# Kernel tuning notes

Measured on AMD Instinct MI355X. Metric: run time of the kernel, lower is better.

The kernel has to match this reference:

```python
import jax, jax.numpy as jnp
import numpy as np

N, H, W = 8, 512, 512
C = 16
TEX = 1024
LEVELS = 4
SH_START = 3


def setup_inputs() -> dict:
    key = jax.random.key(0)
    ks = jax.random.split(key, 2 + LEVELS)
    d = {
        "uv_map": jax.random.uniform(ks[0], (N, H, W, 2), dtype=jnp.float32),
        "sh_basis_map": jax.random.normal(ks[1], (N, H, W, 9), dtype=jnp.float32),
    }
    for i in range(LEVELS):
        s = int(round(TEX / 2.0 ** i))
        d[f"tex{i}"] = jax.random.normal(ks[2 + i], (s, s, C), dtype=jnp.float32) * 0.05
    return d


def _grid_sample_bilinear(tex, uv):
    """torch.grid_sample(mode=bilinear, padding=zeros, align_corners=False),
    grid built as (2u-1, -(2v-1)). tex: [Ht,Wt,C]; uv: [N,H,W,2] in [0,1].
    Returns [N,H,W,C]."""
    Ht, Wt, _ = tex.shape
    gx = uv[..., 0] * 2.0 - 1.0
    gy = -(uv[..., 1] * 2.0 - 1.0)  # y flip from original code
    ix = ((gx + 1.0) * Wt - 1.0) * 0.5  # unnormalize, align_corners=False
    iy = ((gy + 1.0) * Ht - 1.0) * 0.5
    ix0 = jnp.floor(ix); iy0 = jnp.floor(iy)
    ix1 = ix0 + 1.0;     iy1 = iy0 + 1.0
    wx1 = ix - ix0; wx0 = 1.0 - wx1
    wy1 = iy - iy0; wy0 = 1.0 - wy1

    def gather(iyf, ixf):
        iyi = iyf.astype(jnp.int32)
        ixi = ixf.astype(jnp.int32)
        valid = ((iyi >= 0) & (iyi < Ht) & (ixi >= 0) & (ixi < Wt))
        v = tex[jnp.clip(iyi, 0, Ht - 1), jnp.clip(ixi, 0, Wt - 1)]  # [N,H,W,C]
        return v * valid[..., None].astype(tex.dtype)  # zeros padding

    out = (gather(iy0, ix0) * (wy0 * wx0)[..., None]
           + gather(iy0, ix1) * (wy0 * wx1)[..., None]
           + gather(iy1, ix0) * (wy1 * wx0)[..., None]
           + gather(iy1, ix1) * (wy1 * wx1)[..., None])
    return out


def reference(uv_map, sh_basis_map, tex0, tex1, tex2, tex3):
    # accumulate all mipmap levels sampled at the same uv grid
    out = _grid_sample_bilinear(tex0, uv_map)
    for tex in (tex1, tex2, tex3):
        out = out + _grid_sample_bilinear(tex, uv_map)
    # mask pixels where u == 0
    mask = (uv_map[..., 0] == 0.0)[..., None]
    out = jnp.where(mask, 0.0, out)
    # SH multiply on channels [SH_START : SH_START+9]
    out = jnp.concatenate(
        [out[..., :SH_START],
         out[..., SH_START:SH_START + 9] * sh_basis_map,
         out[..., SH_START + 9:]], axis=-1)
    return out.transpose(0, 3, 1, 2)  # [N, C, H, W]
```

## Files before the change

kernel.cpp:

```cpp
#include <hip/hip_runtime.h>

#define NB 8
#define H 512
#define W 512
#define HW (H * W)
#define C 16
#define NPIX (NB * HW)
#define SH_START 3

#define G 32
#define NBINS (G * G)
#define CAP 4096
#define DUMPSLOT (NBINS * CAP)

#define BS_BLOCKS 256
#define BS_THREADS 1024
#define PXB (NPIX / BS_BLOCKS)
#define KPT (PXB / BS_THREADS)

#define OFF_RECS   ((size_t)0)
#define OFF_INTER  ((size_t)67112960)
#define OFF_CUR    ((size_t)134221824)
#define WS_NEED    ((size_t)134225920)

#define TSTR 20
#define LDS0 0
#define LDS1 (1156 * TSTR)
#define LDS2 ((1156 + 324) * TSTR)
#define LDS3 ((1156 + 324 + 100) * TSTR)
#define LDS_FLOATS ((1156 + 324 + 100 + 36) * TSTR)

typedef float f32x4 __attribute__((ext_vector_type(4)));
typedef unsigned int u32x2 __attribute__((ext_vector_type(2)));

__device__ __forceinline__ int bin_of(float u, float v) {
    int bx = (int)(u * (float)G);
    int by = (int)(v * (float)G);
    bx = bx < 0 ? 0 : (bx > G - 1 ? G - 1 : bx);
    by = by < 0 ? 0 : (by > G - 1 ? G - 1 : by);
    return by * G + bx;
}

__device__ __forceinline__ unsigned int f2bf(float f) {
    unsigned int u = __float_as_uint(f);
    unsigned int r = (u + 0x7FFFu + ((u >> 16) & 1u)) >> 16;
    return r & 0xFFFFu;
}

__global__ __launch_bounds__(BS_THREADS) void binsort_kernel(const float* __restrict__ uv,
                                                             int* __restrict__ cur,
                                                             float4* __restrict__ recs) {
    __shared__ f32x4 stage[PXB];
    __shared__ int h[NBINS];
    __shared__ int lstart[NBINS];
    __shared__ int gbase[NBINS];
    int tid = threadIdx.x;
    int pbase = blockIdx.x * PXB;
    const float2* uv2 = reinterpret_cast<const float2*>(uv);

    float2 p[KPT];
    int bn[KPT];
    h[tid] = 0;
    __syncthreads();
#pragma unroll
    for (int k = 0; k < KPT; ++k) {
        p[k] = uv2[pbase + tid + k * BS_THREADS];
        bn[k] = bin_of(p[k].x, p[k].y);
        atomicAdd(&h[bn[k]], 1);
    }
    __syncthreads();
    int cnt = h[tid];
    gbase[tid] = atomicAdd(&cur[tid], cnt);
    lstart[tid] = cnt;
    __syncthreads();
    for (int off = 1; off < NBINS; off <<= 1) {
        int v = (tid >= off) ? lstart[tid - off] : 0;
        __syncthreads();
        lstart[tid] += v;
        __syncthreads();
    }
    int excl = lstart[tid] - cnt;
    __syncthreads();
    lstart[tid] = excl;
    h[tid] = 0;
    __syncthreads();
#pragma unroll
    for (int k = 0; k < KPT; ++k) {
        int b = bn[k];
        int r = atomicAdd(&h[b], 1);
        int ls = lstart[b] + r;
        int within = gbase[b] + r;
        int gs = (within < CAP) ? (b * CAP + within) : DUMPSLOT;
        f32x4 rec;
        rec.x = p[k].x;
        rec.y = p[k].y;
        rec.z = __int_as_float(pbase + tid + k * BS_THREADS);
        rec.w = __int_as_float(gs);
        stage[ls] = rec;
    }
    __syncthreads();
#pragma unroll
    for (int k = 0; k < KPT; ++k) {
        f32x4 rec = stage[tid + k * BS_THREADS];
        int gs = __float_as_int(rec.w);
        __builtin_nontemporal_store(rec, reinterpret_cast<f32x4*>(recs) + gs);
    }
}

template<int S, int N>
__device__ __forceinline__ void stage_mip(const float* __restrict__ t,
                                          float* __restrict__ lbase,
                                          int x0, int y0, int tid) {
    for (int i = tid; i < N * N * 4; i += 1024) {
        int tx = i >> 2, ch = i & 3;
        int ly = tx / N, lx = tx - ly * N;
        int gy = y0 + ly, gx = x0 + lx;
        f32x4 val = {0.0f, 0.0f, 0.0f, 0.0f};
        if (gy >= 0 && gy < S && gx >= 0 && gx < S)
            val = *reinterpret_cast<const f32x4*>(t + ((size_t)(gy * S + gx)) * C + ch * 4);
        *reinterpret_cast<f32x4*>(lbase + (ly * N + lx) * TSTR + ch * 4) = val;
    }
}

template<int S, int N>
__device__ __forceinline__ void sample_mip_lds(const float* __restrict__ lbase,
                                               int x0, int y0,
                                               float u, float v, int ch4, f32x4& acc) {
    float Sf = (float)S;
    float gx = u * 2.0f - 1.0f;
    float gy = -(v * 2.0f - 1.0f);
    float ix = ((gx + 1.0f) * Sf - 1.0f) * 0.5f;
    float iy = ((gy + 1.0f) * Sf - 1.0f) * 0.5f;
    float ix0f = floorf(ix);
    float iy0f = floorf(iy);
    float wx1 = ix - ix0f;
    float wy1 = iy - iy0f;
    float wx0 = 1.0f - wx1;
    float wy0 = 1.0f - wy1;
    int lx = (int)ix0f - x0;
    int ly = (int)iy0f - y0;
    const float* p = lbase + (ly * N + lx) * TSTR + ch4;
    f32x4 t00 = *reinterpret_cast<const f32x4*>(p);
    f32x4 t01 = *reinterpret_cast<const f32x4*>(p + TSTR);
    f32x4 t10 = *reinterpret_cast<const f32x4*>(p + TSTR * N);
    f32x4 t11 = *reinterpret_cast<const f32x4*>(p + TSTR * N + TSTR);
    float w00 = wy0 * wx0, w01 = wy0 * wx1, w10 = wy1 * wx0, w11 = wy1 * wx1;
    acc.x = fmaf(t00.x, w00, acc.x);
    acc.y = fmaf(t00.y, w00, acc.y);
    acc.z = fmaf(t00.z, w00, acc.z);
    acc.w = fmaf(t00.w, w00, acc.w);
    acc.x = fmaf(t01.x, w01, acc.x);
    acc.y = fmaf(t01.y, w01, acc.y);
    acc.z = fmaf(t01.z, w01, acc.z);
    acc.w = fmaf(t01.w, w01, acc.w);
    acc.x = fmaf(t10.x, w10, acc.x);
    acc.y = fmaf(t10.y, w10, acc.y);
    acc.z = fmaf(t10.z, w10, acc.z);
    acc.w = fmaf(t10.w, w10, acc.w);
    acc.x = fmaf(t11.x, w11, acc.x);
    acc.y = fmaf(t11.y, w11, acc.y);
    acc.z = fmaf(t11.z, w11, acc.z);
    acc.w = fmaf(t11.w, w11, acc.w);
}

__global__ __launch_bounds__(1024) void phaseA_kernel(
    const float4* __restrict__ recs, const int* __restrict__ cur,
    const float* __restrict__ t0, const float* __restrict__ t1,
    const float* __restrict__ t2, const float* __restrict__ t3,
    unsigned int* __restrict__ inter) {
    __shared__ float lds[LDS_FLOATS];
    int blk = blockIdx.x;
    int bin = (blk & 7) * (NBINS / 8) + (blk >> 3);
    int bx = bin & (G - 1), by = bin >> 5;
    int tid = threadIdx.x;

    const int x0_0 = bx * 32 - 1, y0_0 = 1024 - (by + 1) * 32 - 1;
    const int x0_1 = bx * 16 - 1, y0_1 = 512  - (by + 1) * 16 - 1;
    const int x0_2 = bx * 8  - 1, y0_2 = 256  - (by + 1) * 8  - 1;
    const int x0_3 = bx * 4  - 1, y0_3 = 128  - (by + 1) * 4  - 1;

    stage_mip<1024, 34>(t0, lds + LDS0, x0_0, y0_0, tid);
    stage_mip<512,  18>(t1, lds + LDS1, x0_1, y0_1, tid);
    stage_mip<256,  10>(t2, lds + LDS2, x0_2, y0_2, tid);
    stage_mip<128,   6>(t3, lds + LDS3, x0_3, y0_3, tid);
    __syncthreads();

    int start = bin * CAP;
    int cnt = cur[bin];
    if (cnt > CAP) cnt = CAP;

    int wave = tid >> 6;
    int lane = tid & 63;
    int q    = lane >> 2;
    int chq  = lane & 3;
    int ch4  = chq * 4;

    for (int i0 = wave * 16; i0 < cnt; i0 += 16 * 16) {
        int i = i0 + q;
        if (i < cnt) {
            float4 r = recs[start + i];
            float u = r.x, v = r.y;
            int pix = __float_as_int(r.z);

            f32x4 acc = {0.0f, 0.0f, 0.0f, 0.0f};
            sample_mip_lds<1024, 34>(lds + LDS0, x0_0, y0_0, u, v, ch4, acc);
            sample_mip_lds<512,  18>(lds + LDS1, x0_1, y0_1, u, v, ch4, acc);
            sample_mip_lds<256,  10>(lds + LDS2, x0_2, y0_2, u, v, ch4, acc);
            sample_mip_lds<128,   6>(lds + LDS3, x0_3, y0_3, u, v, ch4, acc);

            if (u == 0.0f) acc = (f32x4){0.0f, 0.0f, 0.0f, 0.0f};

            u32x2 pk;
            pk.x = f2bf(acc.x) | (f2bf(acc.y) << 16);
            pk.y = f2bf(acc.z) | (f2bf(acc.w) << 16);
            u32x2* op = reinterpret_cast<u32x2*>(inter) + (size_t)pix * 4 + chq;
            __builtin_nontemporal_store(pk, op);
        }
    }
}

__global__ __launch_bounds__(256) void phaseB_kernel(const unsigned int* __restrict__ inter,
                                                     const float* __restrict__ sh,
                                                     float* __restrict__ out) {
    __shared__ float shs[256 * 9];
    int base = blockIdx.x * 256;
    const float* shp = sh + (size_t)base * 9;
    for (int i = threadIdx.x; i < 256 * 9; i += 256) shs[i] = shp[i];
    __syncthreads();

    int pix = base + threadIdx.x;
    const uint4* ip = reinterpret_cast<const uint4*>(inter) + (size_t)pix * 2;
    uint4 a = ip[0];
    uint4 b = ip[1];
#define BLO(x) __uint_as_float((x) << 16)
#define BHI(x) __uint_as_float((x) & 0xFFFF0000u)
    float c0  = BLO(a.x), c1  = BHI(a.x), c2  = BLO(a.y), c3  = BHI(a.y);
    float c4  = BLO(a.z), c5  = BHI(a.z), c6  = BLO(a.w), c7  = BHI(a.w);
    float c8  = BLO(b.x), c9  = BHI(b.x), c10 = BLO(b.y), c11 = BHI(b.y);
    float c12 = BLO(b.z), c13 = BHI(b.z), c14 = BLO(b.w), c15 = BHI(b.w);
#undef BLO
#undef BHI
    const float* s = &shs[threadIdx.x * 9];
    c3  *= s[0];
    c4  *= s[1]; c5  *= s[2]; c6  *= s[3]; c7  *= s[4];
    c8  *= s[5]; c9  *= s[6]; c10 *= s[7]; c11 *= s[8];

    int n  = pix >> 18;
    int hw = pix & (HW - 1);
    float* op = out + (size_t)n * C * HW + hw;
    __builtin_nontemporal_store(c0,  op + 0 * HW);
    __builtin_nontemporal_store(c1,  op + 1 * HW);
    __builtin_nontemporal_store(c2,  op + 2 * HW);
    __builtin_nontemporal_store(c3,  op + 3 * HW);
    __builtin_nontemporal_store(c4,  op + 4 * HW);
    __builtin_nontemporal_store(c5,  op + 5 * HW);
    __builtin_nontemporal_store(c6,  op + 6 * HW);
    __builtin_nontemporal_store(c7,  op + 7 * HW);
    __builtin_nontemporal_store(c8,  op + (size_t)8 * HW);
    __builtin_nontemporal_store(c9,  op + (size_t)9 * HW);
    __builtin_nontemporal_store(c10, op + (size_t)10 * HW);
    __builtin_nontemporal_store(c11, op + (size_t)11 * HW);
    __builtin_nontemporal_store(c12, op + (size_t)12 * HW);
    __builtin_nontemporal_store(c13, op + (size_t)13 * HW);
    __builtin_nontemporal_store(c14, op + (size_t)14 * HW);
    __builtin_nontemporal_store(c15, op + (size_t)15 * HW);
}

__device__ __forceinline__ void tap(const float* __restrict__ t, int S, int iy, int ix,
                                    float w, float acc[C]) {
    if (iy >= 0 && iy < S && ix >= 0 && ix < S) {
        const float4* p = reinterpret_cast<const float4*>(t + ((size_t)iy * S + ix) * C);
        float4 q0 = p[0];
        float4 q1 = p[1];
        float4 q2 = p[2];
        float4 q3 = p[3];
        acc[0]  = fmaf(q0.x, w, acc[0]);
        acc[1]  = fmaf(q0.y, w, acc[1]);
        acc[2]  = fmaf(q0.z, w, acc[2]);
        acc[3]  = fmaf(q0.w, w, acc[3]);
        acc[4]  = fmaf(q1.x, w, acc[4]);
        acc[5]  = fmaf(q1.y, w, acc[5]);
        acc[6]  = fmaf(q1.z, w, acc[6]);
        acc[7]  = fmaf(q1.w, w, acc[7]);
        acc[8]  = fmaf(q2.x, w, acc[8]);
        acc[9]  = fmaf(q2.y, w, acc[9]);
        acc[10] = fmaf(q2.z, w, acc[10]);
        acc[11] = fmaf(q2.w, w, acc[11]);
        acc[12] = fmaf(q3.x, w, acc[12]);
        acc[13] = fmaf(q3.y, w, acc[13]);
        acc[14] = fmaf(q3.z, w, acc[14]);
        acc[15] = fmaf(q3.w, w, acc[15]);
    }
}

__device__ __forceinline__ void sample_level(const float* __restrict__ t, int S,
                                             float u, float v, float acc[C]) {
    float Sf = (float)S;
    float gx = u * 2.0f - 1.0f;
    float gy = -(v * 2.0f - 1.0f);
    float ix = ((gx + 1.0f) * Sf - 1.0f) * 0.5f;
    float iy = ((gy + 1.0f) * Sf - 1.0f) * 0.5f;
    float ix0f = floorf(ix);
    float iy0f = floorf(iy);
    float wx1 = ix - ix0f;
    float wy1 = iy - iy0f;
    float wx0 = 1.0f - wx1;
    float wy0 = 1.0f - wy1;
    int ix0 = (int)ix0f;
    int iy0 = (int)iy0f;
    tap(t, S, iy0,     ix0,     wy0 * wx0, acc);
    tap(t, S, iy0,     ix0 + 1, wy0 * wx1, acc);
    tap(t, S, iy0 + 1, ix0,     wy1 * wx0, acc);
    tap(t, S, iy0 + 1, ix0 + 1, wy1 * wx1, acc);
}

__global__ __launch_bounds__(256) void texmap_kernel(
    const float* __restrict__ uv, const float* __restrict__ sh,
    const float* __restrict__ t0, const float* __restrict__ t1,
    const float* __restrict__ t2, const float* __restrict__ t3,
    float* __restrict__ out) {
    int idx = blockIdx.x * 256 + threadIdx.x;
    if (idx >= NPIX) return;

    float2 uvv = *reinterpret_cast<const float2*>(uv + (size_t)idx * 2);
    float u = uvv.x;
    float v = uvv.y;

    float acc[C];
#pragma unroll
    for (int c = 0; c < C; ++c) acc[c] = 0.0f;

    sample_level(t0, 1024, u, v, acc);
    sample_level(t1, 512,  u, v, acc);
    sample_level(t2, 256,  u, v, acc);
    sample_level(t3, 128,  u, v, acc);

    if (u == 0.0f) {
#pragma unroll
        for (int c = 0; c < C; ++c) acc[c] = 0.0f;
    }

    const float* shp = sh + (size_t)idx * 9;
#pragma unroll
    for (int j = 0; j < 9; ++j) acc[SH_START + j] *= shp[j];

    int n  = idx >> 18;
    int hw = idx & (HW - 1);
    float* op = out + (size_t)n * C * HW + hw;
#pragma unroll
    for (int c = 0; c < C; ++c) {
        __builtin_nontemporal_store(acc[c], op + (size_t)c * HW);
    }
}

extern "C" void kernel_launch(void* const* d_in, const int* in_sizes, int n_in,
                              void* d_out, int out_size, void* d_ws, size_t ws_size,
                              hipStream_t stream) {
    const float* uv = (const float*)d_in[0];
    const float* sh = (const float*)d_in[1];
    const float* t0 = (const float*)d_in[2];
    const float* t1 = (const float*)d_in[3];
    const float* t2 = (const float*)d_in[4];
    const float* t3 = (const float*)d_in[5];
    float* out = (float*)d_out;

    if (ws_size < WS_NEED) {
        texmap_kernel<<<dim3((NPIX + 255) / 256), dim3(256), 0, stream>>>(
            uv, sh, t0, t1, t2, t3, out);
        return;
    }

    char* ws = (char*)d_ws;
    float4*       recs  = (float4*)(ws + OFF_RECS);
    unsigned int* inter = (unsigned int*)(ws + OFF_INTER);
    int*          cur   = (int*)(ws + OFF_CUR);

    (void)hipMemsetAsync(cur, 0, NBINS * sizeof(int), stream);
    binsort_kernel<<<dim3(BS_BLOCKS), dim3(BS_THREADS), 0, stream>>>(uv, cur, recs);
    phaseA_kernel<<<dim3(NBINS), dim3(1024), 0, stream>>>(
        recs, cur, t0, t1, t2, t3, inter);
    phaseB_kernel<<<dim3(NPIX / 256), dim3(256), 0, stream>>>(inter, sh, out);
}
```

Before: 177.6 us.

## Use finer 64x64 UV bins with smaller LDS tiles and 512-thread sampling blocks

Doubles the bin grid resolution to 64x64. Each sampling block now stages a much smaller texture footprint per mip level into shared memory, and uses 512 threads instead of 1024 so more blocks can be resident per CU. The binsort kernel is generalized so each thread handles several bins in the histogram and scan, and it launches twice as many blocks. The trade-off is 4x more bins, more scan work and atomics in binsort, and a lower per-bin capacity of 1024 that risks overflow into the dump slot if bins are uneven.

```diff
diff --git a/kernel.cpp b/kernel.cpp
--- a/kernel.cpp
+++ b/kernel.cpp
@@ -8,12 +8,12 @@
 #define NPIX (NB * HW)
 #define SH_START 3
 
-#define G 32
+#define G 64
 #define NBINS (G * G)
-#define CAP 4096
+#define CAP 1024
 #define DUMPSLOT (NBINS * CAP)
 
-#define BS_BLOCKS 256
+#define BS_BLOCKS 512
 #define BS_THREADS 1024
 #define PXB (NPIX / BS_BLOCKS)
 #define KPT (PXB / BS_THREADS)
@@ -21,14 +21,18 @@
 #define OFF_RECS   ((size_t)0)
 #define OFF_INTER  ((size_t)67112960)
 #define OFF_CUR    ((size_t)134221824)
-#define WS_NEED    ((size_t)134225920)
-
-#define TSTR 20
+#define WS_NEED    ((size_t)134238208)
+
+#define TSTR 16
+#define NT0 18
+#define NT1 10
+#define NT2 6
+#define NT3 4
 #define LDS0 0
-#define LDS1 (1156 * TSTR)
-#define LDS2 ((1156 + 324) * TSTR)
-#define LDS3 ((1156 + 324 + 100) * TSTR)
-#define LDS_FLOATS ((1156 + 324 + 100 + 36) * TSTR)
+#define LDS1 (324 * TSTR)
+#define LDS2 ((324 + 100) * TSTR)
+#define LDS3 ((324 + 100 + 36) * TSTR)
+#define LDS_FLOATS ((324 + 100 + 36 + 16) * TSTR)
 
 typedef float f32x4 __attribute__((ext_vector_type(4)));
 typedef unsigned int u32x2 __attribute__((ext_vector_type(2)));
@@ -60,7 +64,8 @@
 
     float2 p[KPT];
     int bn[KPT];
-    h[tid] = 0;
+#pragma unroll
+    for (int j = 0; j < NBINS / BS_THREADS; ++j) h[tid + j * BS_THREADS] = 0;
     __syncthreads();
 #pragma unroll
     for (int k = 0; k < KPT; ++k) {
@@ -69,20 +74,34 @@
         atomicAdd(&h[bn[k]], 1);
     }
     __syncthreads();
-    int cnt = h[tid];
-    gbase[tid] = atomicAdd(&cur[tid], cnt);
-    lstart[tid] = cnt;
+    int cnt_[NBINS / BS_THREADS];
+#pragma unroll
+    for (int j = 0; j < NBINS / BS_THREADS; ++j) {
+        int b = tid + j * BS_THREADS;
+        cnt_[j] = h[b];
+        gbase[b] = atomicAdd(&cur[b], cnt_[j]);
+        lstart[b] = cnt_[j];
+    }
     __syncthreads();
     for (int off = 1; off < NBINS; off <<= 1) {
-        int v = (tid >= off) ? lstart[tid - off] : 0;
+        int tmp[NBINS / BS_THREADS];
+#pragma unroll
+        for (int j = 0; j < NBINS / BS_THREADS; ++j) {
+            int b = tid + j * BS_THREADS;
+            tmp[j] = (b >= off) ? lstart[b - off] : 0;
+        }
         __syncthreads();
-        lstart[tid] += v;
+#pragma unroll
+        for (int j = 0; j < NBINS / BS_THREADS; ++j)
+            lstart[tid + j * BS_THREADS] += tmp[j];
         __syncthreads();
     }
-    int excl = lstart[tid] - cnt;
-    __syncthreads();
-    lstart[tid] = excl;
-    h[tid] = 0;
+#pragma unroll
+    for (int j = 0; j < NBINS / BS_THREADS; ++j) {
+        int b = tid + j * BS_THREADS;
+        lstart[b] -= cnt_[j];
+        h[b] = 0;
+    }
     __syncthreads();
 #pragma unroll
     for (int k = 0; k < KPT; ++k) {
@@ -111,7 +130,7 @@
 __device__ __forceinline__ void stage_mip(const float* __restrict__ t,
                                           float* __restrict__ lbase,
                                           int x0, int y0, int tid) {
-    for (int i = tid; i < N * N * 4; i += 1024) {
+    for (int i = tid; i < N * N * 4; i += 512) {
         int tx = i >> 2, ch = i & 3;
         int ly = tx / N, lx = tx - ly * N;
         int gy = y0 + ly, gx = x0 + lx;
@@ -163,7 +182,7 @@
     acc.w = fmaf(t11.w, w11, acc.w);
 }
 
-__global__ __launch_bounds__(1024) void phaseA_kernel(
+__global__ __launch_bounds__(512, 8) void phaseA_kernel(
     const float4* __restrict__ recs, const int* __restrict__ cur,
     const float* __restrict__ t0, const float* __restrict__ t1,
     const float* __restrict__ t2, const float* __restrict__ t3,
@@ -171,18 +190,18 @@
     __shared__ float lds[LDS_FLOATS];
     int blk = blockIdx.x;
     int bin = (blk & 7) * (NBINS / 8) + (blk >> 3);
-    int bx = bin & (G - 1), by = bin >> 5;
+    int bx = bin & (G - 1), by = bin >> 6;
     int tid = threadIdx.x;
 
-    const int x0_0 = bx * 32 - 1, y0_0 = 1024 - (by + 1) * 32 - 1;
-    const int x0_1 = bx * 16 - 1, y0_1 = 512  - (by + 1) * 16 - 1;
-    const int x0_2 = bx * 8  - 1, y0_2 = 256  - (by + 1) * 8  - 1;
-    const int x0_3 = bx * 4  - 1, y0_3 = 128  - (by + 1) * 4  - 1;
-
-    stage_mip<1024, 34>(t0, lds + LDS0, x0_0, y0_0, tid);
-    stage_mip<512,  18>(t1, lds + LDS1, x0_1, y0_1, tid);
-    stage_mip<256,  10>(t2, lds + LDS2, x0_2, y0_2, tid);
-    stage_mip<128,   6>(t3, lds + LDS3, x0_3, y0_3, tid);
+    const int x0_0 = bx * 16 - 1, y0_0 = 1024 - (by + 1) * 16 - 1;
+    const int x0_1 = bx * 8  - 1, y0_1 = 512  - (by + 1) * 8  - 1;
+    const int x0_2 = bx * 4  - 1, y0_2 = 256  - (by + 1) * 4  - 1;
+    const int x0_3 = bx * 2  - 1, y0_3 = 128  - (by + 1) * 2  - 1;
+
+    stage_mip<1024, NT0>(t0, lds + LDS0, x0_0, y0_0, tid);
+    stage_mip<512,  NT1>(t1, lds + LDS1, x0_1, y0_1, tid);
+    stage_mip<256,  NT2>(t2, lds + LDS2, x0_2, y0_2, tid);
+    stage_mip<128,  NT3>(t3, lds + LDS3, x0_3, y0_3, tid);
     __syncthreads();
 
     int start = bin * CAP;
@@ -195,7 +214,7 @@
     int chq  = lane & 3;
     int ch4  = chq * 4;
 
-    for (int i0 = wave * 16; i0 < cnt; i0 += 16 * 16) {
+    for (int i0 = wave * 16; i0 < cnt; i0 += 8 * 16) {
         int i = i0 + q;
         if (i < cnt) {
             float4 r = recs[start + i];
@@ -203,10 +222,10 @@
             int pix = __float_as_int(r.z);
 
             f32x4 acc = {0.0f, 0.0f, 0.0f, 0.0f};
-            sample_mip_lds<1024, 34>(lds + LDS0, x0_0, y0_0, u, v, ch4, acc);
-            sample_mip_lds<512,  18>(lds + LDS1, x0_1, y0_1, u, v, ch4, acc);
-            sample_mip_lds<256,  10>(lds + LDS2, x0_2, y0_2, u, v, ch4, acc);
-            sample_mip_lds<128,   6>(lds + LDS3, x0_3, y0_3, u, v, ch4, acc);
+            sample_mip_lds<1024, NT0>(lds + LDS0, x0_0, y0_0, u, v, ch4, acc);
+            sample_mip_lds<512,  NT1>(lds + LDS1, x0_1, y0_1, u, v, ch4, acc);
+            sample_mip_lds<256,  NT2>(lds + LDS2, x0_2, y0_2, u, v, ch4, acc);
+            sample_mip_lds<128,  NT3>(lds + LDS3, x0_3, y0_3, u, v, ch4, acc);
 
             if (u == 0.0f) acc = (f32x4){0.0f, 0.0f, 0.0f, 0.0f};
 
@@ -377,7 +396,7 @@
 
     (void)hipMemsetAsync(cur, 0, NBINS * sizeof(int), stream);
     binsort_kernel<<<dim3(BS_BLOCKS), dim3(BS_THREADS), 0, stream>>>(uv, cur, recs);
-    phaseA_kernel<<<dim3(NBINS), dim3(1024), 0, stream>>>(
+    phaseA_kernel<<<dim3(NBINS), dim3(512), 0, stream>>>(
         recs, cur, t0, t1, t2, t3, inter);
     phaseB_kernel<<<dim3(NPIX / 256), dim3(256), 0, stream>>>(inter, sh, out);
 }
```

Result: slower. 215.4 us (+21.3%).

## Stage mip tiles in LDS as bf16, halve phaseA block size, prefetch records

Applied to the files above, without the earlier changes.

Texture tiles staged into LDS are converted to packed bf16 with an 8-dword texel stride, which halves LDS footprint and read bandwidth. PhaseA blocks drop from 1024 to 512 threads, so more blocks can be resident per CU. The sampling loop is software-pipelined so the next record is loaded while the current one is sampled, and the bin count is read before staging. Quantising the texels to bf16 before interpolation adds precision error on top of the existing bf16 intermediate.

```diff
diff --git a/kernel.cpp b/kernel.cpp
--- a/kernel.cpp
+++ b/kernel.cpp
@@ -23,12 +23,11 @@
 #define OFF_CUR    ((size_t)134221824)
 #define WS_NEED    ((size_t)134225920)
 
-#define TSTR 20
-#define LDS0 0
-#define LDS1 (1156 * TSTR)
-#define LDS2 ((1156 + 324) * TSTR)
-#define LDS3 ((1156 + 324 + 100) * TSTR)
-#define LDS_FLOATS ((1156 + 324 + 100 + 36) * TSTR)
+#define D0 0
+#define D1 (1156 * 8)
+#define D2 ((1156 + 324) * 8)
+#define D3 ((1156 + 324 + 100) * 8)
+#define LDS_DWORDS ((1156 + 324 + 100 + 36) * 8)
 
 typedef float f32x4 __attribute__((ext_vector_type(4)));
 typedef unsigned int u32x2 __attribute__((ext_vector_type(2)));
@@ -108,24 +107,30 @@
 }
 
 template<int S, int N>
-__device__ __forceinline__ void stage_mip(const float* __restrict__ t,
-                                          float* __restrict__ lbase,
-                                          int x0, int y0, int tid) {
-    for (int i = tid; i < N * N * 4; i += 1024) {
+__device__ __forceinline__ void stage_mip_bf16(const float* __restrict__ t,
+                                               unsigned int* __restrict__ lbase,
+                                               int x0, int y0, int tid) {
+    for (int i = tid; i < N * N * 4; i += 512) {
         int tx = i >> 2, ch = i & 3;
         int ly = tx / N, lx = tx - ly * N;
         int gy = y0 + ly, gx = x0 + lx;
-        f32x4 val = {0.0f, 0.0f, 0.0f, 0.0f};
-        if (gy >= 0 && gy < S && gx >= 0 && gx < S)
-            val = *reinterpret_cast<const f32x4*>(t + ((size_t)(gy * S + gx)) * C + ch * 4);
-        *reinterpret_cast<f32x4*>(lbase + (ly * N + lx) * TSTR + ch * 4) = val;
-    }
-}
+        u32x2 d = {0u, 0u};
+        if (gy >= 0 && gy < S && gx >= 0 && gx < S) {
+            f32x4 val = *reinterpret_cast<const f32x4*>(t + ((size_t)(gy * S + gx)) * C + ch * 4);
+            d.x = f2bf(val.x) | (f2bf(val.y) << 16);
+            d.y = f2bf(val.z) | (f2bf(val.w) << 16);
+        }
+        *reinterpret_cast<u32x2*>(lbase + (ly * N + lx) * 8 + ch * 2) = d;
+    }
+}
+
+#define BFL(x) __uint_as_float((x) << 16)
+#define BFH(x) __uint_as_float((x) & 0xFFFF0000u)
 
 template<int S, int N>
-__device__ __forceinline__ void sample_mip_lds(const float* __restrict__ lbase,
-                                               int x0, int y0,
-                                               float u, float v, int ch4, f32x4& acc) {
+__device__ __forceinline__ void sample_mip_bf16(const unsigned int* __restrict__ lbase,
+                                                int x0, int y0,
+                                                float u, float v, int ch2, f32x4& acc) {
     float Sf = (float)S;
     float gx = u * 2.0f - 1.0f;
     float gy = -(v * 2.0f - 1.0f);
@@ -139,83 +144,95 @@
     float wy0 = 1.0f - wy1;
     int lx = (int)ix0f - x0;
     int ly = (int)iy0f - y0;
-    const float* p = lbase + (ly * N + lx) * TSTR + ch4;
-    f32x4 t00 = *reinterpret_cast<const f32x4*>(p);
-    f32x4 t01 = *reinterpret_cast<const f32x4*>(p + TSTR);
-    f32x4 t10 = *reinterpret_cast<const f32x4*>(p + TSTR * N);
-    f32x4 t11 = *reinterpret_cast<const f32x4*>(p + TSTR * N + TSTR);
+    const unsigned int* p = lbase + (ly * N + lx) * 8 + ch2;
+    u32x2 d00 = *reinterpret_cast<const u32x2*>(p);
+    u32x2 d01 = *reinterpret_cast<const u32x2*>(p + 8);
+    u32x2 d10 = *reinterpret_cast<const u32x2*>(p + 8 * N);
+    u32x2 d11 = *reinterpret_cast<const u32x2*>(p + 8 * N + 8);
     float w00 = wy0 * wx0, w01 = wy0 * wx1, w10 = wy1 * wx0, w11 = wy1 * wx1;
-    acc.x = fmaf(t00.x, w00, acc.x);
-    acc.y = fmaf(t00.y, w00, acc.y);
-    acc.z = fmaf(t00.z, w00, acc.z);
-    acc.w = fmaf(t00.w, w00, acc.w);
-    acc.x = fmaf(t01.x, w01, acc.x);
-    acc.y = fmaf(t01.y, w01, acc.y);
-    acc.z = fmaf(t01.z, w01, acc.z);
-    acc.w = fmaf(t01.w, w01, acc.w);
-    acc.x = fmaf(t10.x, w10, acc.x);
-    acc.y = fmaf(t10.y, w10, acc.y);
-    acc.z = fmaf(t10.z, w10, acc.z);
-    acc.w = fmaf(t10.w, w10, acc.w);
-    acc.x = fmaf(t11.x, w11, acc.x);
-    acc.y = fmaf(t11.y, w11, acc.y);
-    acc.z = fmaf(t11.z, w11, acc.z);
-    acc.w = fmaf(t11.w, w11, acc.w);
-}
-
-__global__ __launch_bounds__(1024) void phaseA_kernel(
+    acc.x = fmaf(BFL(d00.x), w00, acc.x);
+    acc.y = fmaf(BFH(d00.x), w00, acc.y);
+    acc.z = fmaf(BFL(d00.y), w00, acc.z);
+    acc.w = fmaf(BFH(d00.y), w00, acc.w);
+    acc.x = fmaf(BFL(d01.x), w01, acc.x);
+    acc.y = fmaf(BFH(d01.x), w01, acc.y);
+    acc.z = fmaf(BFL(d01.y), w01, acc.z);
+    acc.w = fmaf(BFH(d01.y), w01, acc.w);
+    acc.x = fmaf(BFL(d10.x), w10, acc.x);
+    acc.y = fmaf(BFH(d10.x), w10, acc.y);
+    acc.z = fmaf(BFL(d10.y), w10, acc.z);
+    acc.w = fmaf(BFH(d10.y), w10, acc.w);
+    acc.x = fmaf(BFL(d11.x), w11, acc.x);
+    acc.y = fmaf(BFH(d11.x), w11, acc.y);
+    acc.z = fmaf(BFL(d11.y), w11, acc.z);
+    acc.w = fmaf(BFH(d11.y), w11, acc.w);
+}
+
+__global__ __launch_bounds__(512) void phaseA_kernel(
     const float4* __restrict__ recs, const int* __restrict__ cur,
     const float* __restrict__ t0, const float* __restrict__ t1,
     const float* __restrict__ t2, const float* __restrict__ t3,
     unsigned int* __restrict__ inter) {
-    __shared__ float lds[LDS_FLOATS];
+    __shared__ unsigned int lds[LDS_DWORDS];
     int blk = blockIdx.x;
     int bin = (blk & 7) * (NBINS / 8) + (blk >> 3);
     int bx = bin & (G - 1), by = bin >> 5;
     int tid = threadIdx.x;
 
+    int cnt = cur[bin];
+    if (cnt > CAP) cnt = CAP;
+    int start = bin * CAP;
+
     const int x0_0 = bx * 32 - 1, y0_0 = 1024 - (by + 1) * 32 - 1;
     const int x0_1 = bx * 16 - 1, y0_1 = 512  - (by + 1) * 16 - 1;
     const int x0_2 = bx * 8  - 1, y0_2 = 256  - (by + 1) * 8  - 1;
     const int x0_3 = bx * 4  - 1, y0_3 = 128  - (by + 1) * 4  - 1;
 
-    stage_mip<1024, 34>(t0, lds + LDS0, x0_0, y0_0, tid);
-    stage_mip<512,  18>(t1, lds + LDS1, x0_1, y0_1, tid);
-    stage_mip<256,  10>(t2, lds + LDS2, x0_2, y0_2, tid);
-    stage_mip<128,   6>(t3, lds + LDS3, x0_3, y0_3, tid);
-    __syncthreads();
-
-    int start = bin * CAP;
-    int cnt = cur[bin];
-    if (cnt > CAP) cnt = CAP;
+    stage_mip_bf16<1024, 34>(t0, lds + D0, x0_0, y0_0, tid);
+    stage_mip_bf16<512,  18>(t1, lds + D1, x0_1, y0_1, tid);
+    stage_mip_bf16<256,  10>(t2, lds + D2, x0_2, y0_2, tid);
+    stage_mip_bf16<128,   6>(t3, lds + D3, x0_3, y0_3, tid);
+    __syncthreads();
 
     int wave = tid >> 6;
     int lane = tid & 63;
     int q    = lane >> 2;
     int chq  = lane & 3;
-    int ch4  = chq * 4;
-
-    for (int i0 = wave * 16; i0 < cnt; i0 += 16 * 16) {
-        int i = i0 + q;
-        if (i < cnt) {
-            float4 r = recs[start + i];
-            float u = r.x, v = r.y;
-            int pix = __float_as_int(r.z);
-
-            f32x4 acc = {0.0f, 0.0f, 0.0f, 0.0f};
-            sample_mip_lds<1024, 34>(lds + LDS0, x0_0, y0_0, u, v, ch4, acc);
-            sample_mip_lds<512,  18>(lds + LDS1, x0_1, y0_1, u, v, ch4, acc);
-            sample_mip_lds<256,  10>(lds + LDS2, x0_2, y0_2, u, v, ch4, acc);
-            sample_mip_lds<128,   6>(lds + LDS3, x0_3, y0_3, u, v, ch4, acc);
-
-            if (u == 0.0f) acc = (f32x4){0.0f, 0.0f, 0.0f, 0.0f};
-
+    int ch2  = chq * 2;
+
+    if (cnt <= 0) return;
+
+    int i0 = wave * 16;
+    int cm1 = cnt - 1;
+    int i = i0 + q;
+    float4 r = recs[start + (i < cm1 ? i : cm1)];
+    while (i0 < cnt) {
+        int ni0 = i0 + 8 * 16;
+        float4 rn = r;
+        if (ni0 < cnt) {
+            int ni = ni0 + q;
+            rn = recs[start + (ni < cm1 ? ni : cm1)];
+        }
+        float u = r.x, v = r.y;
+        int pix = __float_as_int(r.z);
+
+        f32x4 acc = {0.0f, 0.0f, 0.0f, 0.0f};
+        sample_mip_bf16<1024, 34>(lds + D0, x0_0, y0_0, u, v, ch2, acc);
+        sample_mip_bf16<512,  18>(lds + D1, x0_1, y0_1, u, v, ch2, acc);
+        sample_mip_bf16<256,  10>(lds + D2, x0_2, y0_2, u, v, ch2, acc);
+        sample_mip_bf16<128,   6>(lds + D3, x0_3, y0_3, u, v, ch2, acc);
+
+        if (u == 0.0f) acc = (f32x4){0.0f, 0.0f, 0.0f, 0.0f};
+
+        if (i0 + q < cnt) {
             u32x2 pk;
             pk.x = f2bf(acc.x) | (f2bf(acc.y) << 16);
             pk.y = f2bf(acc.z) | (f2bf(acc.w) << 16);
             u32x2* op = reinterpret_cast<u32x2*>(inter) + (size_t)pix * 4 + chq;
             __builtin_nontemporal_store(pk, op);
         }
+        r = rn;
+        i0 = ni0;
     }
 }
 
@@ -232,14 +249,10 @@
     const uint4* ip = reinterpret_cast<const uint4*>(inter) + (size_t)pix * 2;
     uint4 a = ip[0];
     uint4 b = ip[1];
-#define BLO(x) __uint_as_float((x) << 16)
-#define BHI(x) __uint_as_float((x) & 0xFFFF0000u)
-    float c0  = BLO(a.x), c1  = BHI(a.x), c2  = BLO(a.y), c3  = BHI(a.y);
-    float c4  = BLO(a.z), c5  = BHI(a.z), c6  = BLO(a.w), c7  = BHI(a.w);
-    float c8  = BLO(b.x), c9  = BHI(b.x), c10 = BLO(b.y), c11 = BHI(b.y);
-    float c12 = BLO(b.z), c13 = BHI(b.z), c14 = BLO(b.w), c15 = BHI(b.w);
-#undef BLO
-#undef BHI
+    float c0  = BFL(a.x), c1  = BFH(a.x), c2  = BFL(a.y), c3  = BFH(a.y);
+    float c4  = BFL(a.z), c5  = BFH(a.z), c6  = BFL(a.w), c7  = BFH(a.w);
+    float c8  = BFL(b.x), c9  = BFH(b.x), c10 = BFL(b.y), c11 = BFH(b.y);
+    float c12 = BFL(b.z), c13 = BFH(b.z), c14 = BFL(b.w), c15 = BFH(b.w);
     const float* s = &shs[threadIdx.x * 9];
     c3  *= s[0];
     c4  *= s[1]; c5  *= s[2]; c6  *= s[3]; c7  *= s[4];
@@ -377,7 +390,7 @@
 
     (void)hipMemsetAsync(cur, 0, NBINS * sizeof(int), stream);
     binsort_kernel<<<dim3(BS_BLOCKS), dim3(BS_THREADS), 0, stream>>>(uv, cur, recs);
-    phaseA_kernel<<<dim3(NBINS), dim3(1024), 0, stream>>>(
+    phaseA_kernel<<<dim3(NBINS), dim3(512), 0, stream>>>(
         recs, cur, t0, t1, t2, t3, inter);
     phaseB_kernel<<<dim3(NPIX / 256), dim3(256), 0, stream>>>(inter, sh, out);
 }
```

Result: no change. 176.6 us (-0.6%).
